# Performance work log

Measured on AMD Instinct MI355X. Metric: run time of the kernel, lower is better.

Reference implementation:

```python
import jax, jax.numpy as jnp
import numpy as np

EMBED_DIM = 2048
HEAD_DIM = 128            # __init__ head_dim arg
HALF = HEAD_DIM // 2      # internal self.head_dim = 64
NH2 = EMBED_DIM // HALF   # 32 q/k heads
H = NH2 // 2              # 16 differential heads
DEPTH = 12
LAMBDA_INIT = 0.8 - 0.6 * float(np.exp(-0.3 * DEPTH))
SCALING = HEAD_DIM ** (-0.5)   # source divides scores by this (== *sqrt(head_dim))
BATCH, SEQ = 1, 2048
EPS = 1e-5


def setup_inputs() -> dict:
    key = jax.random.key(0)
    ks = jax.random.split(key, 10)
    wstd = 0.25 / float(np.sqrt(EMBED_DIM))  # keep logits moderate despite *sqrt(head_dim)
    return {
        "x": jax.random.normal(ks[0], (BATCH, SEQ, EMBED_DIM), jnp.float32),
        "wq": jax.random.normal(ks[1], (EMBED_DIM, EMBED_DIM), jnp.float32) * wstd,
        "wk": jax.random.normal(ks[2], (EMBED_DIM, EMBED_DIM), jnp.float32) * wstd,
        "wv": jax.random.normal(ks[3], (EMBED_DIM, EMBED_DIM), jnp.float32) * wstd,
        "wout": jax.random.normal(ks[4], (EMBED_DIM, EMBED_DIM), jnp.float32) * wstd,
        "lambda_q1": jax.random.normal(ks[5], (HALF,), jnp.float32) * 0.1,
        "lambda_q2": jax.random.normal(ks[6], (HALF,), jnp.float32) * 0.1,
        "lambda_k1": jax.random.normal(ks[7], (HALF,), jnp.float32) * 0.1,
        "lambda_k2": jax.random.normal(ks[8], (HALF,), jnp.float32) * 0.1,
        "subln_weight": jnp.ones((2 * HALF,), jnp.float32),
    }


def _rope_tables(t, dim):
    # precompute_freqs_cis: freqs = 1/theta^(arange(0,dim,2)/dim); angles = outer(t, freqs)
    inv = 1.0 / (10000.0 ** (np.arange(0, dim, 2)[: dim // 2].astype(np.float64) / dim))
    ang = np.outer(np.arange(t), inv)
    return jnp.asarray(np.cos(ang), jnp.float32), jnp.asarray(np.sin(ang), jnp.float32)


def _apply_rope(x, cos, sin):
    # x: [b, t, h, d]; interleaved (even, odd) pairs form complex numbers
    xr, xi = x[..., 0::2], x[..., 1::2]
    c = cos[None, :, None, :]
    s = sin[None, :, None, :]
    out = jnp.stack([xr * c - xi * s, xr * s + xi * c], axis=-1)
    return out.reshape(x.shape)


def reference(x, wq, wk, wv, wout, lambda_q1, lambda_q2, lambda_k1, lambda_k2, subln_weight):
    b, t, e = x.shape
    # nn.Linear(bias=False): y = x @ W^T
    q = (x @ wq.T).reshape(b, t, NH2, HALF)
    k = (x @ wk.T).reshape(b, t, NH2, HALF)
    v = (x @ wv.T).reshape(b, t, H, 2 * HALF)  # intended DIFF-attn layout
    cos, sin = _rope_tables(t, HALF)
    q = _apply_rope(q, cos, sin)
    k = _apply_rope(k, cos, sin)
    q = q.transpose(0, 2, 1, 3)  # [b, 2H, t, HALF]
    k = k.transpose(0, 2, 1, 3)
    v = v.transpose(0, 2, 1, 3)  # [b, H, t, 2*HALF]
    # source: attn_weights = qk / scaling  (scaling = head_dim**-0.5 -> multiply by sqrt(head_dim))
    scores = jnp.einsum('bhtd,bhsd->bhts', q, k) / SCALING
    # default attn_mask = triu(zeros) == all zeros -> no masking applied
    probs = jax.nn.softmax(scores, axis=-1)
    lam1 = jnp.exp(jnp.sum(lambda_q1 * lambda_k1))
    lam2 = jnp.exp(jnp.sum(lambda_q2 * lambda_k2))
    lam = lam1 - lam2 + LAMBDA_INIT
    probs = probs.reshape(b, H, 2, t, t)
    diff = probs[:, :, 0] - lam * probs[:, :, 1]        # [b, H, t, t]
    attn = jnp.einsum('bhts,bhsd->bhtd', diff, v)        # [b, H, t, 2*HALF]
    # RMSNorm(2*HALF, eps=1e-5)
    attn = attn * jax.lax.rsqrt(jnp.mean(attn * attn, axis=-1, keepdims=True) + EPS)
    attn = attn * subln_weight
    attn = attn.transpose(0, 2, 1, 3).reshape(b, t, e)
    return attn @ wout.T
```

## Files before the change

kernel.cpp:

```cpp
#include <hip/hip_runtime.h>
#include <math.h>

#define SEQ 2048
#define EMB 2048

typedef _Float16 f16;
typedef unsigned short ushort_t;
typedef __attribute__((ext_vector_type(2))) _Float16 f16x2;
typedef __attribute__((ext_vector_type(4))) _Float16 f16x4;
typedef __attribute__((ext_vector_type(8))) _Float16 f16x8;
typedef __attribute__((ext_vector_type(4))) float f32x4;
typedef __attribute__((ext_vector_type(16))) float f32x16;
typedef __attribute__((ext_vector_type(8))) short bf16x8;
typedef __attribute__((ext_vector_type(4))) unsigned short us4;
typedef __attribute__((ext_vector_type(8))) unsigned short us8;
typedef __attribute__((ext_vector_type(4))) unsigned int uint4v;

__device__ __forceinline__ void gload16(const void* g, void* l) {
  __builtin_amdgcn_global_load_lds((const __attribute__((address_space(1))) unsigned int*)g,
                                   (__attribute__((address_space(3))) unsigned int*)l, 16, 0, 0);
}

__device__ __forceinline__ ushort_t f32_to_bf16(float f) {
  unsigned int u = __builtin_bit_cast(unsigned int, f);
  u += 0x7FFFu + ((u >> 16) & 1u);
  return (ushort_t)(u >> 16);
}

__device__ __forceinline__ unsigned cvt_pk_bf16_2(float lo, float hi) {
  unsigned r;
  asm("v_cvt_pk_bf16_f32 %0, %1, %2" : "=v"(r) : "v"(lo), "v"(hi));
  return r;
}

__global__ __launch_bounds__(256) void cvt5_kernel(const float* __restrict__ i0,
                                                   const float* __restrict__ i1,
                                                   const float* __restrict__ i2,
                                                   const float* __restrict__ i3,
                                                   const float* __restrict__ i4,
                                                   f16* __restrict__ o0, f16* __restrict__ o1,
                                                   f16* __restrict__ o2, f16* __restrict__ o3,
                                                   f16* __restrict__ o4) {
  int b = blockIdx.x;
  int z = b >> 12;
  const float* in = (z == 0) ? i0 : (z == 1) ? i1 : (z == 2) ? i2 : (z == 3) ? i3 : i4;
  f16* out = (z == 0) ? o0 : (z == 1) ? o1 : (z == 2) ? o2 : (z == 3) ? o3 : o4;
  int i = ((b & 4095) * 256 + threadIdx.x) * 4;
  f32x4 v = *(const f32x4*)(in + i);
  *(f16x4*)(out + i) = __builtin_convertvector(v, f16x4);
}

__global__ __launch_bounds__(256) void rope_table_kernel(float* __restrict__ cosT,
                                                         float* __restrict__ sinT) {
  int id = blockIdx.x * 256 + threadIdx.x;
  int t = id >> 5, i = id & 31;
  double inv = pow(10000.0, -(double)i / 32.0);
  double ang = (double)t * inv;
  cosT[id] = (float)cos(ang);
  sinT[id] = (float)sin(ang);
}

__global__ __launch_bounds__(256, 3) void proj_gemm_kernel(
    const f16* __restrict__ A, const f16* __restrict__ B0, const f16* __restrict__ B1,
    const f16* __restrict__ B2, const float* __restrict__ cosT, const float* __restrict__ sinT,
    f16* __restrict__ qout, f16* __restrict__ kout, ushort_t* __restrict__ vtout) {
  const int z = blockIdx.z;
  const f16* __restrict__ B = (z == 0) ? B0 : ((z == 1) ? B1 : B2);
  __shared__ f16 As[128 * 32];
  __shared__ f16 Bs[128 * 32];
  const int tid = threadIdx.x;
  const int wave = tid >> 6, lane = tid & 63;
  const int l16 = lane & 15, quad = lane >> 4;
  const int wm = (wave >> 1) << 6, wn = (wave & 1) << 6;
  const int bm = blockIdx.y << 7, bn = blockIdx.x << 7;

  const int swg = ((lane & 3) ^ ((lane >> 3) & 3)) * 8;
  const f16* Ag = A + (size_t)(bm + wave * 32 + (lane >> 2)) * EMB + swg;
  const f16* Bg = B + (size_t)(bn + wave * 32 + (lane >> 2)) * EMB + swg;
  f16* Asl = &As[wave * 1024 + lane * 8];
  f16* Bsl = &Bs[wave * 1024 + lane * 8];

  const int swr = (quad ^ ((l16 >> 1) & 3)) * 8;
  int aoff[4], boff[4];
#pragma unroll
  for (int i = 0; i < 4; i++) {
    aoff[i] = (wm + i * 16 + l16) * 32 + swr;
    boff[i] = (wn + i * 16 + l16) * 32 + swr;
  }

  f32x4 acc[4][4];
#pragma unroll
  for (int i = 0; i < 4; i++)
#pragma unroll
    for (int j = 0; j < 4; j++) acc[i][j] = (f32x4){0.f, 0.f, 0.f, 0.f};

  for (int k0 = 0; k0 < EMB; k0 += 32) {
    __syncthreads();
    gload16(Ag + k0, Asl);
    gload16(Ag + (size_t)16 * EMB + k0, Asl + 512);
    gload16(Bg + k0, Bsl);
    gload16(Bg + (size_t)16 * EMB + k0, Bsl + 512);
    __syncthreads();
    f16x8 af[4], bf[4];
#pragma unroll
    for (int mi = 0; mi < 4; mi++) af[mi] = *(const f16x8*)&As[aoff[mi]];
#pragma unroll
    for (int ni = 0; ni < 4; ni++) bf[ni] = *(const f16x8*)&Bs[boff[ni]];
#pragma unroll
    for (int mi = 0; mi < 4; mi++)
#pragma unroll
      for (int ni = 0; ni < 4; ni++)
        acc[mi][ni] = __builtin_amdgcn_mfma_f32_16x16x32_f16(af[mi], bf[ni], acc[mi][ni], 0, 0, 0);
  }

  if (z == 2) {
#pragma unroll
    for (int mi = 0; mi < 4; mi++) {
#pragma unroll
      for (int ni = 0; ni < 4; ni++) {
        int row0 = bm + wm + mi * 16 + quad * 4;
        int col = bn + wn + ni * 16 + l16;
        us4 o;
#pragma unroll
        for (int rg = 0; rg < 4; rg++) o[rg] = f32_to_bf16(acc[mi][ni][rg]);
        int hidx = col >> 7, d = col & 127, t = row0;
        size_t idx = ((((size_t)hidx * 32 + (t >> 6)) * 4 + ((t >> 4) & 3)) * 4 + (d >> 5)) * 512 +
                     (((t >> 3) & 1) * 32 + (d & 31)) * 8 + (t & 7);
        *(us4*)&vtout[idx] = o;
      }
    }
  } else {
    f16* Co = (z == 0) ? qout : kout;
    const float scale = (z == 0) ? 16.3222307f : 1.0f;
#pragma unroll
    for (int mi = 0; mi < 4; mi++) {
#pragma unroll
      for (int ni = 0; ni < 4; ni++) {
        int row0 = bm + wm + mi * 16 + quad * 4;
        int col = bn + wn + ni * 16 + l16;
        int i_r = (col & 63) >> 1;
        int odd = col & 1;
#pragma unroll
        for (int rg = 0; rg < 4; rg++) {
          int t = row0 + rg;
          float c = cosT[(t << 5) + i_r] * scale;
          float s = sinT[(t << 5) + i_r] * scale;
          float own = acc[mi][ni][rg];
          float other = __shfl_xor(own, 1);
          float xr = odd ? other : own;
          float xi = odd ? own : other;
          float outv = odd ? (xr * s + xi * c) : (xr * c - xi * s);
          Co[(size_t)t * EMB + col] = (f16)outv;
        }
      }
    }
  }
}

__global__ __launch_bounds__(256, 2) void out_gemm_kernel(const f16* __restrict__ A,
                                                          const f16* __restrict__ B,
                                                          float* __restrict__ C) {
  __shared__ f16 As[128 * 32];
  __shared__ f16 Bs[64 * 32];
  const int tid = threadIdx.x;
  const int wave = tid >> 6, lane = tid & 63;
  const int l16 = lane & 15, quad = lane >> 4;
  const int wm = (wave >> 1) << 6, wn = (wave & 1) << 5;
  const int bm = blockIdx.y << 7, bn = blockIdx.x << 6;

  const int swg = ((lane & 3) ^ ((lane >> 3) & 3)) * 8;
  const f16* Ag = A + (size_t)(bm + wave * 32 + (lane >> 2)) * EMB + swg;
  const f16* Bg = B + (size_t)(bn + wave * 16 + (lane >> 2)) * EMB + swg;
  f16* Asl = &As[wave * 1024 + lane * 8];
  f16* Bsl = &Bs[wave * 512 + lane * 8];

  const int swr = (quad ^ ((l16 >> 1) & 3)) * 8;
  int aoff[4], boff[2];
#pragma unroll
  for (int i = 0; i < 4; i++) aoff[i] = (wm + i * 16 + l16) * 32 + swr;
#pragma unroll
  for (int i = 0; i < 2; i++) boff[i] = (wn + i * 16 + l16) * 32 + swr;

  f32x4 acc[4][2];
#pragma unroll
  for (int i = 0; i < 4; i++)
#pragma unroll
    for (int j = 0; j < 2; j++) acc[i][j] = (f32x4){0.f, 0.f, 0.f, 0.f};

  for (int k0 = 0; k0 < EMB; k0 += 32) {
    __syncthreads();
    gload16(Ag + k0, Asl);
    gload16(Ag + (size_t)16 * EMB + k0, Asl + 512);
    gload16(Bg + k0, Bsl);
    __syncthreads();
    f16x8 af[4], bf[2];
#pragma unroll
    for (int mi = 0; mi < 4; mi++) af[mi] = *(const f16x8*)&As[aoff[mi]];
#pragma unroll
    for (int ni = 0; ni < 2; ni++) bf[ni] = *(const f16x8*)&Bs[boff[ni]];
#pragma unroll
    for (int mi = 0; mi < 4; mi++)
#pragma unroll
      for (int ni = 0; ni < 2; ni++)
        acc[mi][ni] = __builtin_amdgcn_mfma_f32_16x16x32_f16(af[mi], bf[ni], acc[mi][ni], 0, 0, 0);
  }

#pragma unroll
  for (int mi = 0; mi < 4; mi++) {
#pragma unroll
    for (int ni = 0; ni < 2; ni++) {
      int row0 = bm + wm + mi * 16 + quad * 4;
      int col = bn + wn + ni * 16 + l16;
#pragma unroll
      for (int rg = 0; rg < 4; rg++)
        C[(size_t)(row0 + rg) * EMB + col] = acc[mi][ni][rg];
    }
  }
}

__global__ __launch_bounds__(256, 2) void diff_attn_v9(
    const f16* __restrict__ qb, const f16* __restrict__ kb, const ushort_t* __restrict__ vbT,
    const float* __restrict__ lq1, const float* __restrict__ lq2,
    const float* __restrict__ lk1, const float* __restrict__ lk2,
    const float* __restrict__ subw, f16* __restrict__ attnb) {
  const int h = blockIdx.x;
  const int qblk = blockIdx.y;
  const int tid = threadIdx.x;
  const int wave = tid >> 6, lane = tid & 63;
  const int l32 = lane & 31, hi = lane >> 5;
  const int hh = wave >> 1, qs = wave & 1;

  __shared__ f16 Ks[2][8192];
  __shared__ ushort_t Vt[2][8192];

  const int qrow0 = qblk * 64 + qs * 32;
  f16x8 qf[4];
#pragma unroll
  for (int c = 0; c < 4; c++)
    qf[c] = *(const f16x8*)(qb + (size_t)(qrow0 + l32) * EMB + h * 128 + hh * 64 + c * 16 + hi * 8);

  f32x16 O[4];
#pragma unroll
  for (int dt = 0; dt < 4; dt++)
#pragma unroll
    for (int s2 = 0; s2 < 16; s2++) O[dt][s2] = 0.f;
  float lsum = 0.f;

  const int hhs = wave >> 1, kbs = wave & 1;
  const f16* kgp = kb + (size_t)(kbs * 32 + l32) * EMB + h * 128 + hhs * 64 + hi * 8;
  const ushort_t* vgp = vbT + ((size_t)h * 32) * 8192 + (size_t)wave * 2048 + lane * 8;

  auto stage = [&](int buf, int it) {
#pragma unroll
    for (int j2 = 0; j2 < 4; j2++)
      gload16(kgp + (size_t)it * (64 * EMB) + j2 * 16, &Ks[buf][(wave * 4 + j2) * 512]);
#pragma unroll
    for (int j2 = 0; j2 < 4; j2++)
      gload16(vgp + (size_t)it * 8192 + j2 * 512, &Vt[buf][(wave * 4 + j2) * 512]);
  };

  stage(0, 0);
  __syncthreads();

  auto qk4 = [&](const f16* KsC, int kbi) {
    f32x16 acc;
#pragma unroll
    for (int s2 = 0; s2 < 16; s2++) acc[s2] = -28.8539008f;
#pragma unroll
    for (int c = 0; c < 4; c++) {
      f16x8 kf = *(const f16x8*)&KsC[(hh * 8 + kbi * 4 + c) * 512 + lane * 8];
      acc = __builtin_amdgcn_mfma_f32_32x32x16_f16(kf, qf[c], acc, 0, 0, 0);
    }
    return acc;
  };

  auto exppack = [&](const f32x16& acc, bf16x8* pf2) {
    float p[16];
#pragma unroll
    for (int s2 = 0; s2 < 16; s2++) p[s2] = __builtin_exp2f(acc[s2]);
    lsum += (((p[0] + p[1]) + (p[2] + p[3])) + ((p[4] + p[5]) + (p[6] + p[7]))) +
            (((p[8] + p[9]) + (p[10] + p[11])) + ((p[12] + p[13]) + (p[14] + p[15])));
#pragma unroll
    for (int c2 = 0; c2 < 2; c2++) {
      unsigned w0 = cvt_pk_bf16_2(p[8 * c2 + 0], p[8 * c2 + 1]);
      unsigned w1 = cvt_pk_bf16_2(p[8 * c2 + 2], p[8 * c2 + 3]);
      unsigned w2 = cvt_pk_bf16_2(p[8 * c2 + 4], p[8 * c2 + 5]);
      unsigned w3 = cvt_pk_bf16_2(p[8 * c2 + 6], p[8 * c2 + 7]);
      asm("v_permlane32_swap_b32 %0, %1" : "+v"(w0), "+v"(w2));
      asm("v_permlane32_swap_b32 %0, %1" : "+v"(w1), "+v"(w3));
      uint4v pw;
      pw.x = w0; pw.y = w1; pw.z = w2; pw.w = w3;
      pf2[c2] = __builtin_bit_cast(bf16x8, pw);
    }
  };

  auto pv2 = [&](const ushort_t* VtC, int kc0, const bf16x8* pf2) {
#pragma unroll
    for (int c2 = 0; c2 < 2; c2++) {
#pragma unroll
      for (int dt = 0; dt < 4; dt++) {
        bf16x8 vf = *(const bf16x8*)&VtC[((kc0 + c2) * 4 + dt) * 512 + lane * 8];
        O[dt] = __builtin_amdgcn_mfma_f32_32x32x16_bf16(vf, pf2[c2], O[dt], 0, 0, 0);
      }
    }
  };

  auto step = [&](int cbuf, int nit) {
    if (nit < 32) stage(cbuf ^ 1, nit);

    const f16* KsC = &Ks[cbuf][0];
    const ushort_t* VtC = &Vt[cbuf][0];

    f32x16 acc0 = qk4(KsC, 0);
    f32x16 acc1 = qk4(KsC, 1);
    bf16x8 pfa[2], pfb[2];
    exppack(acc0, pfa);
    __builtin_amdgcn_s_setprio(1);
    pv2(VtC, 0, pfa);
    __builtin_amdgcn_s_setprio(0);
    exppack(acc1, pfb);
    __builtin_amdgcn_s_setprio(1);
    pv2(VtC, 2, pfb);
    __builtin_amdgcn_s_setprio(0);
    __syncthreads();
  };

  for (int it = 0; it < 32; it += 2) {
    step(0, it + 1);
    step(1, it + 2);
  }

  float d1 = 0.f, d2 = 0.f;
  for (int i = 0; i < 64; i++) {
    d1 += lq1[i] * lk1[i];
    d2 += lq2[i] * lk2[i];
  }
  const float lam = __expf(d1) - __expf(d2) + 0.783605767f;

  float s = lsum + __shfl_xor(lsum, 32);
  const float inv = (hh == 0) ? (1.f / s) : (lam / s);

  float* Obuf = (float*)&Ks[0][0];
  if (hh == 1) {
#pragma unroll
    for (int dt = 0; dt < 4; dt++)
#pragma unroll
      for (int rq = 0; rq < 4; rq++) {
        f32x4 v;
#pragma unroll
        for (int rg = 0; rg < 4; rg++) v[rg] = O[dt][rq * 4 + rg] * inv;
        *(f32x4*)&Obuf[(((qs * 4 + dt) * 4 + rq) * 64 + lane) * 4] = v;
      }
  }
  __syncthreads();
  if (hh == 0) {
    float a[4][16];
    float ms = 0.f;
#pragma unroll
    for (int dt = 0; dt < 4; dt++)
#pragma unroll
      for (int rq = 0; rq < 4; rq++) {
        f32x4 o1 = *(const f32x4*)&Obuf[(((qs * 4 + dt) * 4 + rq) * 64 + lane) * 4];
#pragma unroll
        for (int rg = 0; rg < 4; rg++) {
          float v = O[dt][rq * 4 + rg] * inv - o1[rg];
          a[dt][rq * 4 + rg] = v;
          ms += v * v;
        }
      }
    ms += __shfl_xor(ms, 32);
    const float rms = rsqrtf(ms * (1.f / 128.f) + 1e-5f);
    const int t_g = qrow0 + l32;
#pragma unroll
    for (int dt = 0; dt < 4; dt++)
#pragma unroll
      for (int rq = 0; rq < 4; rq++) {
        f32x4 sw = *(const f32x4*)(subw + dt * 32 + rq * 8 + hi * 4);
        f16x4 o;
#pragma unroll
        for (int rg = 0; rg < 4; rg++) o[rg] = (f16)(a[dt][rq * 4 + rg] * rms * sw[rg]);
        *(f16x4*)(attnb + (size_t)t_g * EMB + h * 128 + dt * 32 + rq * 8 + hi * 4) = o;
      }
  }
}

extern "C" void kernel_launch(void* const* d_in, const int* in_sizes, int n_in,
                              void* d_out, int out_size, void* d_ws, size_t ws_size,
                              hipStream_t stream) {
  const float* x    = (const float*)d_in[0];
  const float* wq   = (const float*)d_in[1];
  const float* wk   = (const float*)d_in[2];
  const float* wv   = (const float*)d_in[3];
  const float* wout = (const float*)d_in[4];
  const float* lq1  = (const float*)d_in[5];
  const float* lq2  = (const float*)d_in[6];
  const float* lk1  = (const float*)d_in[7];
  const float* lk2  = (const float*)d_in[8];
  const float* subw = (const float*)d_in[9];
  float* out = (float*)d_out;

  char* ws = (char*)d_ws;
  const size_t MB = 1024 * 1024;
  f16* xb    = (f16*)(ws + 0 * MB);
  f16* wqb   = (f16*)(ws + 8 * MB);
  f16* wkb   = (f16*)(ws + 16 * MB);
  f16* wvb   = (f16*)(ws + 24 * MB);
  f16* woutb = (f16*)(ws + 32 * MB);
  f16* qb    = (f16*)(ws + 40 * MB);
  f16* kb    = (f16*)(ws + 48 * MB);
  ushort_t* vbT = (ushort_t*)(ws + 56 * MB);
  f16* attnb = (f16*)(ws + 64 * MB);
  float* cosT = (float*)(ws + 72 * MB);
  float* sinT = (float*)(ws + 72 * MB + 262144);

  dim3 b256(256);
  cvt5_kernel<<<5 * 4096, b256, 0, stream>>>(x, wq, wk, wv, wout, xb, wqb, wkb, wvb, woutb);
  rope_table_kernel<<<256, b256, 0, stream>>>(cosT, sinT);

  proj_gemm_kernel<<<dim3(16, 16, 3), b256, 0, stream>>>(xb, wqb, wkb, wvb, cosT, sinT, qb, kb,
                                                         vbT);

  diff_attn_v9<<<dim3(16, 32), b256, 0, stream>>>(qb, kb, vbT, lq1, lq2, lk1, lk2, subw, attnb);

  out_gemm_kernel<<<dim3(32, 16), b256, 0, stream>>>(attnb, woutb, out);
}
```

Before: 296.8 us.

## Multi-buffer async loads in projection GEMM and diff-attention with vmcnt waits

```diff
diff --git a/kernel.cpp b/kernel.cpp
--- a/kernel.cpp
+++ b/kernel.cpp
@@ -66,8 +66,8 @@
     f16* __restrict__ qout, f16* __restrict__ kout, ushort_t* __restrict__ vtout) {
   const int z = blockIdx.z;
   const f16* __restrict__ B = (z == 0) ? B0 : ((z == 1) ? B1 : B2);
-  __shared__ f16 As[128 * 32];
-  __shared__ f16 Bs[128 * 32];
+  __shared__ f16 As[3 * 4096];
+  __shared__ f16 Bs[3 * 4096];
   const int tid = threadIdx.x;
   const int wave = tid >> 6, lane = tid & 63;
   const int l16 = lane & 15, quad = lane >> 4;
@@ -77,8 +77,7 @@
   const int swg = ((lane & 3) ^ ((lane >> 3) & 3)) * 8;
   const f16* Ag = A + (size_t)(bm + wave * 32 + (lane >> 2)) * EMB + swg;
   const f16* Bg = B + (size_t)(bn + wave * 32 + (lane >> 2)) * EMB + swg;
-  f16* Asl = &As[wave * 1024 + lane * 8];
-  f16* Bsl = &Bs[wave * 1024 + lane * 8];
+  const int sl = wave * 1024 + lane * 8;
 
   const int swr = (quad ^ ((l16 >> 1) & 3)) * 8;
   int aoff[4], boff[4];
@@ -94,24 +93,39 @@
 #pragma unroll
     for (int j = 0; j < 4; j++) acc[i][j] = (f32x4){0.f, 0.f, 0.f, 0.f};
 
-  for (int k0 = 0; k0 < EMB; k0 += 32) {
-    __syncthreads();
-    gload16(Ag + k0, Asl);
-    gload16(Ag + (size_t)16 * EMB + k0, Asl + 512);
-    gload16(Bg + k0, Bsl);
-    gload16(Bg + (size_t)16 * EMB + k0, Bsl + 512);
-    __syncthreads();
+  auto stage = [&](int b, int it) {
+    int k0 = it * 32;
+    gload16(Ag + k0, &As[b * 4096 + sl]);
+    gload16(Ag + (size_t)16 * EMB + k0, &As[b * 4096 + sl + 512]);
+    gload16(Bg + k0, &Bs[b * 4096 + sl]);
+    gload16(Bg + (size_t)16 * EMB + k0, &Bs[b * 4096 + sl + 512]);
+  };
+  auto compute = [&](int b) {
     f16x8 af[4], bf[4];
 #pragma unroll
-    for (int mi = 0; mi < 4; mi++) af[mi] = *(const f16x8*)&As[aoff[mi]];
-#pragma unroll
-    for (int ni = 0; ni < 4; ni++) bf[ni] = *(const f16x8*)&Bs[boff[ni]];
+    for (int mi = 0; mi < 4; mi++) af[mi] = *(const f16x8*)&As[b * 4096 + aoff[mi]];
+#pragma unroll
+    for (int ni = 0; ni < 4; ni++) bf[ni] = *(const f16x8*)&Bs[b * 4096 + boff[ni]];
 #pragma unroll
     for (int mi = 0; mi < 4; mi++)
 #pragma unroll
       for (int ni = 0; ni < 4; ni++)
         acc[mi][ni] = __builtin_amdgcn_mfma_f32_16x16x32_f16(af[mi], bf[ni], acc[mi][ni], 0, 0, 0);
-  }
+  };
+
+  stage(0, 0);
+  stage(1, 1);
+  for (int it = 0; it < 63; ++it) {
+    asm volatile("s_waitcnt vmcnt(4)" ::: "memory");
+    __builtin_amdgcn_s_barrier();
+    __builtin_amdgcn_sched_barrier(0);
+    compute(it % 3);
+    if (it < 62) stage((it + 2) % 3, it + 2);
+  }
+  asm volatile("s_waitcnt vmcnt(0)" ::: "memory");
+  __builtin_amdgcn_s_barrier();
+  __builtin_amdgcn_sched_barrier(0);
+  compute(63 % 3);
 
   if (z == 2) {
 #pragma unroll
@@ -218,7 +232,7 @@
   }
 }
 
-__global__ __launch_bounds__(256, 2) void diff_attn_v9(
+__global__ __launch_bounds__(256, 2) void diff_attn_v10(
     const f16* __restrict__ qb, const f16* __restrict__ kb, const ushort_t* __restrict__ vbT,
     const float* __restrict__ lq1, const float* __restrict__ lq2,
     const float* __restrict__ lk1, const float* __restrict__ lk2,
@@ -230,8 +244,8 @@
   const int l32 = lane & 31, hi = lane >> 5;
   const int hh = wave >> 1, qs = wave & 1;
 
-  __shared__ f16 Ks[2][8192];
-  __shared__ ushort_t Vt[2][8192];
+  __shared__ f16 KsA[4 * 4096];
+  __shared__ ushort_t VtA[4 * 4096];
 
   const int qrow0 = qblk * 64 + qs * 32;
   f16x8 qf[4];
@@ -246,40 +260,38 @@
     for (int s2 = 0; s2 < 16; s2++) O[dt][s2] = 0.f;
   float lsum = 0.f;
 
-  const int hhs = wave >> 1, kbs = wave & 1;
-  const f16* kgp = kb + (size_t)(kbs * 32 + l32) * EMB + h * 128 + hhs * 64 + hi * 8;
-  const ushort_t* vgp = vbT + ((size_t)h * 32) * 8192 + (size_t)wave * 2048 + lane * 8;
-
-  auto stage = [&](int buf, int it) {
-#pragma unroll
-    for (int j2 = 0; j2 < 4; j2++)
-      gload16(kgp + (size_t)it * (64 * EMB) + j2 * 16, &Ks[buf][(wave * 4 + j2) * 512]);
-#pragma unroll
-    for (int j2 = 0; j2 < 4; j2++)
-      gload16(vgp + (size_t)it * 8192 + j2 * 512, &Vt[buf][(wave * 4 + j2) * 512]);
+  const int T0 = 2 * wave;
+  const f16* kgp = kb + (size_t)l32 * EMB + h * 128 + (T0 >> 2) * 64 + (T0 & 3) * 16 + hi * 8;
+  const ushort_t* vgp = vbT + (size_t)h * 262144 + wave * 1024 + lane * 8;
+
+  auto stage = [&](int b, int it) {
+    const f16* ks = kgp + (size_t)it * 32 * EMB;
+    f16* kd = &KsA[b * 4096 + wave * 1024 + lane * 8];
+    gload16(ks, kd);
+    gload16(ks + 16, kd + 512);
+    const ushort_t* vs = vgp + (it >> 1) * 8192 + (it & 1) * 4096;
+    ushort_t* vd = &VtA[b * 4096 + wave * 1024 + lane * 8];
+    gload16(vs, vd);
+    gload16(vs + 512, vd + 512);
   };
 
-  stage(0, 0);
-  __syncthreads();
-
-  auto qk4 = [&](const f16* KsC, int kbi) {
+  auto compute = [&](int b) {
+    const f16* KsC = &KsA[b * 4096];
+    const ushort_t* VtC = &VtA[b * 4096];
     f32x16 acc;
 #pragma unroll
     for (int s2 = 0; s2 < 16; s2++) acc[s2] = -28.8539008f;
 #pragma unroll
     for (int c = 0; c < 4; c++) {
-      f16x8 kf = *(const f16x8*)&KsC[(hh * 8 + kbi * 4 + c) * 512 + lane * 8];
+      f16x8 kf = *(const f16x8*)&KsC[(hh * 4 + c) * 512 + lane * 8];
       acc = __builtin_amdgcn_mfma_f32_32x32x16_f16(kf, qf[c], acc, 0, 0, 0);
     }
-    return acc;
-  };
-
-  auto exppack = [&](const f32x16& acc, bf16x8* pf2) {
     float p[16];
 #pragma unroll
     for (int s2 = 0; s2 < 16; s2++) p[s2] = __builtin_exp2f(acc[s2]);
     lsum += (((p[0] + p[1]) + (p[2] + p[3])) + ((p[4] + p[5]) + (p[6] + p[7]))) +
             (((p[8] + p[9]) + (p[10] + p[11])) + ((p[12] + p[13]) + (p[14] + p[15])));
+    bf16x8 pf[2];
 #pragma unroll
     for (int c2 = 0; c2 < 2; c2++) {
       unsigned w0 = cvt_pk_bf16_2(p[8 * c2 + 0], p[8 * c2 + 1]);
@@ -290,45 +302,38 @@
       asm("v_permlane32_swap_b32 %0, %1" : "+v"(w1), "+v"(w3));
       uint4v pw;
       pw.x = w0; pw.y = w1; pw.z = w2; pw.w = w3;
-      pf2[c2] = __builtin_bit_cast(bf16x8, pw);
-    }
+      pf[c2] = __builtin_bit_cast(bf16x8, pw);
+    }
+    __builtin_amdgcn_s_setprio(1);
+#pragma unroll
+    for (int c2 = 0; c2 < 2; c2++) {
+#pragma unroll
+      for (int dt = 0; dt < 4; dt++) {
+        bf16x8 vf = *(const bf16x8*)&VtC[(c2 * 4 + dt) * 512 + lane * 8];
+        O[dt] = __builtin_amdgcn_mfma_f32_32x32x16_bf16(vf, pf[c2], O[dt], 0, 0, 0);
+      }
+    }
+    __builtin_amdgcn_s_setprio(0);
   };
 
-  auto pv2 = [&](const ushort_t* VtC, int kc0, const bf16x8* pf2) {
-#pragma unroll
-    for (int c2 = 0; c2 < 2; c2++) {
-#pragma unroll
-      for (int dt = 0; dt < 4; dt++) {
-        bf16x8 vf = *(const bf16x8*)&VtC[((kc0 + c2) * 4 + dt) * 512 + lane * 8];
-        O[dt] = __builtin_amdgcn_mfma_f32_32x32x16_bf16(vf, pf2[c2], O[dt], 0, 0, 0);
-      }
-    }
-  };
-
-  auto step = [&](int cbuf, int nit) {
-    if (nit < 32) stage(cbuf ^ 1, nit);
-
-    const f16* KsC = &Ks[cbuf][0];
-    const ushort_t* VtC = &Vt[cbuf][0];
-
-    f32x16 acc0 = qk4(KsC, 0);
-    f32x16 acc1 = qk4(KsC, 1);
-    bf16x8 pfa[2], pfb[2];
-    exppack(acc0, pfa);
-    __builtin_amdgcn_s_setprio(1);
-    pv2(VtC, 0, pfa);
-    __builtin_amdgcn_s_setprio(0);
-    exppack(acc1, pfb);
-    __builtin_amdgcn_s_setprio(1);
-    pv2(VtC, 2, pfb);
-    __builtin_amdgcn_s_setprio(0);
-    __syncthreads();
-  };
-
-  for (int it = 0; it < 32; it += 2) {
-    step(0, it + 1);
-    step(1, it + 2);
-  }
+  stage(0, 0);
+  stage(1, 1);
+  stage(2, 2);
+  for (int it = 0; it < 62; ++it) {
+    asm volatile("s_waitcnt vmcnt(8)" ::: "memory");
+    __builtin_amdgcn_s_barrier();
+    __builtin_amdgcn_sched_barrier(0);
+    compute(it & 3);
+    if (it < 61) stage((it + 3) & 3, it + 3);
+  }
+  asm volatile("s_waitcnt vmcnt(4)" ::: "memory");
+  __builtin_amdgcn_s_barrier();
+  __builtin_amdgcn_sched_barrier(0);
+  compute(62 & 3);
+  asm volatile("s_waitcnt vmcnt(0)" ::: "memory");
+  __builtin_amdgcn_s_barrier();
+  __builtin_amdgcn_sched_barrier(0);
+  compute(63 & 3);
 
   float d1 = 0.f, d2 = 0.f;
   for (int i = 0; i < 64; i++) {
@@ -340,7 +345,9 @@
   float s = lsum + __shfl_xor(lsum, 32);
   const float inv = (hh == 0) ? (1.f / s) : (lam / s);
 
-  float* Obuf = (float*)&Ks[0][0];
+  __syncthreads();
+
+  float* Obuf = (float*)&KsA[0];
   if (hh == 1) {
 #pragma unroll
     for (int dt = 0; dt < 4; dt++)
@@ -420,7 +427,7 @@
   proj_gemm_kernel<<<dim3(16, 16, 3), b256, 0, stream>>>(xb, wqb, wkb, wvb, cosT, sinT, qb, kb,
                                                          vbT);
 
-  diff_attn_v9<<<dim3(16, 32), b256, 0, stream>>>(qb, kb, vbT, lq1, lq2, lk1, lk2, subw, attnb);
+  diff_attn_v10<<<dim3(16, 32), b256, 0, stream>>>(qb, kb, vbT, lq1, lq2, lk1, lk2, subw, attnb);
 
   out_gemm_kernel<<<dim3(32, 16), b256, 0, stream>>>(attnb, woutb, out);
 }
```

New measurement: 306.1 us. +3.1%, slower.

## Store Q/K in MFMA fragment layout and stream K/V directly into registers

Applied to the files above, without the earlier changes.

```diff
diff --git a/kernel.cpp b/kernel.cpp
--- a/kernel.cpp
+++ b/kernel.cpp
@@ -140,6 +140,7 @@
         int col = bn + wn + ni * 16 + l16;
         int i_r = (col & 63) >> 1;
         int odd = col & 1;
+        int hidx = col >> 7, d = col & 127;
 #pragma unroll
         for (int rg = 0; rg < 4; rg++) {
           int t = row0 + rg;
@@ -150,7 +151,9 @@
           float xr = odd ? other : own;
           float xi = odd ? own : other;
           float outv = odd ? (xr * s + xi * c) : (xr * c - xi * s);
-          Co[(size_t)t * EMB + col] = (f16)outv;
+          size_t idx = ((size_t)((hidx * 64 + (t >> 5)) * 8 + (d >> 4))) * 512 +
+                       ((t & 31) + ((d >> 3) & 1) * 32) * 8 + (d & 7);
+          Co[idx] = (f16)outv;
         }
       }
     }
@@ -218,8 +221,8 @@
   }
 }
 
-__global__ __launch_bounds__(256, 2) void diff_attn_v9(
-    const f16* __restrict__ qb, const f16* __restrict__ kb, const ushort_t* __restrict__ vbT,
+__global__ __launch_bounds__(256, 2) void diff_attn_v11(
+    const f16* __restrict__ qbT, const f16* __restrict__ kbT, const ushort_t* __restrict__ vbT,
     const float* __restrict__ lq1, const float* __restrict__ lq2,
     const float* __restrict__ lk1, const float* __restrict__ lk2,
     const float* __restrict__ subw, f16* __restrict__ attnb) {
@@ -230,14 +233,15 @@
   const int l32 = lane & 31, hi = lane >> 5;
   const int hh = wave >> 1, qs = wave & 1;
 
-  __shared__ f16 Ks[2][8192];
-  __shared__ ushort_t Vt[2][8192];
+  __shared__ float Obuf[8192];
 
   const int qrow0 = qblk * 64 + qs * 32;
   f16x8 qf[4];
-#pragma unroll
-  for (int c = 0; c < 4; c++)
-    qf[c] = *(const f16x8*)(qb + (size_t)(qrow0 + l32) * EMB + h * 128 + hh * 64 + c * 16 + hi * 8);
+  {
+    const f16* qT = qbT + ((size_t)((h * 64 + qblk * 2 + qs) * 8 + hh * 4)) * 512 + lane * 8;
+#pragma unroll
+    for (int c = 0; c < 4; c++) qf[c] = *(const f16x8*)(qT + c * 512);
+  }
 
   f32x16 O[4];
 #pragma unroll
@@ -246,40 +250,33 @@
     for (int s2 = 0; s2 < 16; s2++) O[dt][s2] = 0.f;
   float lsum = 0.f;
 
-  const int hhs = wave >> 1, kbs = wave & 1;
-  const f16* kgp = kb + (size_t)(kbs * 32 + l32) * EMB + h * 128 + hhs * 64 + hi * 8;
-  const ushort_t* vgp = vbT + ((size_t)h * 32) * 8192 + (size_t)wave * 2048 + lane * 8;
-
-  auto stage = [&](int buf, int it) {
-#pragma unroll
-    for (int j2 = 0; j2 < 4; j2++)
-      gload16(kgp + (size_t)it * (64 * EMB) + j2 * 16, &Ks[buf][(wave * 4 + j2) * 512]);
-#pragma unroll
-    for (int j2 = 0; j2 < 4; j2++)
-      gload16(vgp + (size_t)it * 8192 + j2 * 512, &Vt[buf][(wave * 4 + j2) * 512]);
+  const f16* kT = kbT + ((size_t)(h * 64) * 8 + hh * 4) * 512 + lane * 8;
+  const ushort_t* vT = vbT + (size_t)h * 262144 + lane * 8;
+
+  auto loadK = [&](f16x8(&kr)[4], int it) {
+    const f16* p = kT + (size_t)it * 4096;
+#pragma unroll
+    for (int c = 0; c < 4; c++) kr[c] = *(const f16x8*)(p + c * 512);
   };
-
-  stage(0, 0);
-  __syncthreads();
-
-  auto qk4 = [&](const f16* KsC, int kbi) {
+  auto loadV = [&](us8(&vr)[8], int it) {
+    const ushort_t* p = vT + (size_t)it * 4096;
+#pragma unroll
+    for (int T = 0; T < 8; T++) vr[T] = *(const us8*)(p + T * 512);
+  };
+
+  auto compute = [&](const f16x8(&kr)[4], const us8(&vr)[8]) {
     f32x16 acc;
 #pragma unroll
     for (int s2 = 0; s2 < 16; s2++) acc[s2] = -28.8539008f;
 #pragma unroll
-    for (int c = 0; c < 4; c++) {
-      f16x8 kf = *(const f16x8*)&KsC[(hh * 8 + kbi * 4 + c) * 512 + lane * 8];
-      acc = __builtin_amdgcn_mfma_f32_32x32x16_f16(kf, qf[c], acc, 0, 0, 0);
-    }
-    return acc;
-  };
-
-  auto exppack = [&](const f32x16& acc, bf16x8* pf2) {
+    for (int c = 0; c < 4; c++)
+      acc = __builtin_amdgcn_mfma_f32_32x32x16_f16(kr[c], qf[c], acc, 0, 0, 0);
     float p[16];
 #pragma unroll
     for (int s2 = 0; s2 < 16; s2++) p[s2] = __builtin_exp2f(acc[s2]);
     lsum += (((p[0] + p[1]) + (p[2] + p[3])) + ((p[4] + p[5]) + (p[6] + p[7]))) +
             (((p[8] + p[9]) + (p[10] + p[11])) + ((p[12] + p[13]) + (p[14] + p[15])));
+    bf16x8 pf[2];
 #pragma unroll
     for (int c2 = 0; c2 < 2; c2++) {
       unsigned w0 = cvt_pk_bf16_2(p[8 * c2 + 0], p[8 * c2 + 1]);
@@ -290,44 +287,37 @@
       asm("v_permlane32_swap_b32 %0, %1" : "+v"(w1), "+v"(w3));
       uint4v pw;
       pw.x = w0; pw.y = w1; pw.z = w2; pw.w = w3;
-      pf2[c2] = __builtin_bit_cast(bf16x8, pw);
-    }
+      pf[c2] = __builtin_bit_cast(bf16x8, pw);
+    }
+    __builtin_amdgcn_s_setprio(1);
+#pragma unroll
+    for (int c2 = 0; c2 < 2; c2++) {
+#pragma unroll
+      for (int dt = 0; dt < 4; dt++) {
+        bf16x8 vf = __builtin_bit_cast(bf16x8, vr[c2 * 4 + dt]);
+        O[dt] = __builtin_amdgcn_mfma_f32_32x32x16_bf16(vf, pf[c2], O[dt], 0, 0, 0);
+      }
+    }
+    __builtin_amdgcn_s_setprio(0);
   };
 
-  auto pv2 = [&](const ushort_t* VtC, int kc0, const bf16x8* pf2) {
-#pragma unroll
-    for (int c2 = 0; c2 < 2; c2++) {
-#pragma unroll
-      for (int dt = 0; dt < 4; dt++) {
-        bf16x8 vf = *(const bf16x8*)&VtC[((kc0 + c2) * 4 + dt) * 512 + lane * 8];
-        O[dt] = __builtin_amdgcn_mfma_f32_32x32x16_bf16(vf, pf2[c2], O[dt], 0, 0, 0);
-      }
-    }
-  };
-
-  auto step = [&](int cbuf, int nit) {
-    if (nit < 32) stage(cbuf ^ 1, nit);
-
-    const f16* KsC = &Ks[cbuf][0];
-    const ushort_t* VtC = &Vt[cbuf][0];
-
-    f32x16 acc0 = qk4(KsC, 0);
-    f32x16 acc1 = qk4(KsC, 1);
-    bf16x8 pfa[2], pfb[2];
-    exppack(acc0, pfa);
-    __builtin_amdgcn_s_setprio(1);
-    pv2(VtC, 0, pfa);
-    __builtin_amdgcn_s_setprio(0);
-    exppack(acc1, pfb);
-    __builtin_amdgcn_s_setprio(1);
-    pv2(VtC, 2, pfb);
-    __builtin_amdgcn_s_setprio(0);
-    __syncthreads();
-  };
-
-  for (int it = 0; it < 32; it += 2) {
-    step(0, it + 1);
-    step(1, it + 2);
+  f16x8 kA[4], kB[4];
+  us8 vA[8], vB[8];
+  loadK(kA, 0);
+  loadV(vA, 0);
+  loadK(kB, 1);
+  loadV(vB, 1);
+  for (int it = 0; it < 64; it += 2) {
+    compute(kA, vA);
+    if (it + 2 < 64) {
+      loadK(kA, it + 2);
+      loadV(vA, it + 2);
+    }
+    compute(kB, vB);
+    if (it + 3 < 64) {
+      loadK(kB, it + 3);
+      loadV(vB, it + 3);
+    }
   }
 
   float d1 = 0.f, d2 = 0.f;
@@ -340,7 +330,6 @@
   float s = lsum + __shfl_xor(lsum, 32);
   const float inv = (hh == 0) ? (1.f / s) : (lam / s);
 
-  float* Obuf = (float*)&Ks[0][0];
   if (hh == 1) {
 #pragma unroll
     for (int dt = 0; dt < 4; dt++)
@@ -406,8 +395,8 @@
   f16* wkb   = (f16*)(ws + 16 * MB);
   f16* wvb   = (f16*)(ws + 24 * MB);
   f16* woutb = (f16*)(ws + 32 * MB);
-  f16* qb    = (f16*)(ws + 40 * MB);
-  f16* kb    = (f16*)(ws + 48 * MB);
+  f16* qbT   = (f16*)(ws + 40 * MB);
+  f16* kbT   = (f16*)(ws + 48 * MB);
   ushort_t* vbT = (ushort_t*)(ws + 56 * MB);
   f16* attnb = (f16*)(ws + 64 * MB);
   float* cosT = (float*)(ws + 72 * MB);
@@ -417,10 +406,11 @@
   cvt5_kernel<<<5 * 4096, b256, 0, stream>>>(x, wq, wk, wv, wout, xb, wqb, wkb, wvb, woutb);
   rope_table_kernel<<<256, b256, 0, stream>>>(cosT, sinT);
 
-  proj_gemm_kernel<<<dim3(16, 16, 3), b256, 0, stream>>>(xb, wqb, wkb, wvb, cosT, sinT, qb, kb,
+  proj_gemm_kernel<<<dim3(16, 16, 3), b256, 0, stream>>>(xb, wqb, wkb, wvb, cosT, sinT, qbT, kbT,
                                                          vbT);
 
-  diff_attn_v9<<<dim3(16, 32), b256, 0, stream>>>(qb, kb, vbT, lq1, lq2, lk1, lk2, subw, attnb);
+  diff_attn_v11<<<dim3(16, 32), b256, 0, stream>>>(qbT, kbT, vbT, lq1, lq2, lk1, lk2, subw,
+                                                   attnb);
 
   out_gemm_kernel<<<dim3(32, 16), b256, 0, stream>>>(attnb, woutb, out);
 }
```

Measured after the change: 296.0 us. About the same (-0.3%).
